# Kernel tuning notes

Measured on AMD Instinct MI355X. Metric: run time of the kernel, lower is better.

## Reference

```python
import jax, jax.numpy as jnp
import numpy as np

WIN = 11          # win_size
NC = 2            # num_classes
SMOOTH = 0.1      # smoothing / (num_classes - 1) = 0.1/1; fix_flag=True and 0.1 <= Max_Smootning=0.2


def setup_inputs() -> dict:
    key = jax.random.key(0)
    k1, k2 = jax.random.split(key)
    x = jax.random.normal(k1, (8, 2, 1024, 1024), dtype=jnp.float32)
    target = jax.random.randint(k2, (8, 1, 1024, 1024), 0, 2, dtype=jnp.int32)
    return {"x": x, "target": target}


def reference(x, target):
    kern = -jnp.ones((1, 1, WIN, WIN), dtype=jnp.float32)
    kern = kern.at[0, 0, WIN // 2, WIN // 2].set(float(WIN * WIN - 1))

    tf = target.astype(jnp.float32)  # [B,1,H,W]
    pad = WIN // 2
    edge = jax.lax.conv_general_dilated(tf, kern, window_strides=(1, 1),
                                        padding=[(pad, pad), (pad, pad)])
    edge = jnp.where(edge != 0, 1.0, 0.0)  # [B,1,H,W], 1 near label edges

    log_p = jax.nn.log_softmax(x, axis=1)  # [B,C,H,W]

    # One-hot masks (to_categorical with alpha=0 and alpha=smoothing).
    oh = jax.nn.one_hot(target[:, 0], NC, dtype=jnp.float32)  # [B,H,W,C]
    oh = jnp.transpose(oh, (0, 3, 1, 2))                      # [B,C,H,W]
    # alpha everywhere, 1 - alpha + alpha/NC at the true class
    soft = SMOOTH + oh * (1.0 - 2.0 * SMOOTH + SMOOTH / NC)

    mask = oh * (1.0 - edge) + soft * edge  # hard label off-edge, smoothed on-edge
    loss = jnp.mean(jnp.sum(mask * log_p, axis=1))
    return -loss
```

## Files before the change

### kernel.cpp

```cpp
#include <hip/hip_runtime.h>

#define HH 1024
#define WW 1024
#define BB 8
#define WORDS_X 16
#define NPART 2048

typedef unsigned long long u64;

__global__ __launch_bounds__(256) void ls_pack(const int* __restrict__ tgt,
                                               u64* __restrict__ bits) {
    const int lane = threadIdx.x & 63;
    const size_t wv = ((size_t)blockIdx.x * 256 + threadIdx.x) >> 6;
    const size_t wbase = wv * 8;
    const int* p = tgt + wbase * 64 + lane;

    int v[8];
#pragma unroll
    for (int j = 0; j < 8; ++j) v[j] = p[j * 64];

    u64 mine = 0;
#pragma unroll
    for (int j = 0; j < 8; ++j) {
        u64 m = __ballot(v[j] != 0);
        if (lane == j) mine = m;
    }
    if (lane < 8) bits[wbase + lane] = mine;
}

__global__ __launch_bounds__(256) void ls_loss(const float* __restrict__ x,
                                               const u64* __restrict__ bits,
                                               float* __restrict__ partial) {
    __shared__ u64 s_w[74][3];
    __shared__ u64 s_oh[74], s_ah[74], s_e[64];
    __shared__ float s_red[4];

    const int tid = threadIdx.x;
    const int b  = blockIdx.z;
    const int ty = blockIdx.y * 64;
    const int wx = blockIdx.x;

    if (tid < 222) {
        int r = tid / 3, k = tid - 3 * r;
        int gy = ty - 5 + r;
        int wi = wx - 1 + k;
        u64 v = 0;
        if ((unsigned)gy < HH && (unsigned)wi < WORDS_X)
            v = bits[((size_t)(b << 10) + gy) * WORDS_X + wi];
        s_w[r][k] = v;
    }

    const int row = tid >> 2;
    const int c0  = (tid & 3) << 4;
    const float* x0p = x + ((size_t)b * 2 + 0) * HH * WW
                         + (size_t)(ty + row) * WW + (wx << 6) + c0;
    const float* x1p = x0p + (size_t)HH * WW;
    float4 xv0[4], xv1[4];
#pragma unroll
    for (int q = 0; q < 4; ++q) xv0[q] = ((const float4*)x0p)[q];
#pragma unroll
    for (int q = 0; q < 4; ++q) xv1[q] = ((const float4*)x1p)[q];

    __syncthreads();

    if (tid < 74) {
        u64 wl = s_w[tid][0], wm = s_w[tid][1], wr = s_w[tid][2];
        u64 oh = wm, ah = wm;
#pragma unroll
        for (int d = 1; d <= 5; ++d) {
            u64 vr = (wm >> d) | (wr << (64 - d));
            u64 vl = (wm << d) | (wl >> (64 - d));
            oh |= vr | vl;
            ah &= vr & vl;
        }
        s_oh[tid] = oh;
        s_ah[tid] = ah;
    }
    __syncthreads();

    if (tid < 64) {
        u64 ov = 0, av = ~0ULL;
#pragma unroll
        for (int k = 0; k < 11; ++k) { ov |= s_oh[tid + k]; av &= s_ah[tid + k]; }
        u64 tc = s_w[tid + 5][1];
        s_e[tid] = (ov & ~tc) | (~av & tc);
    }
    __syncthreads();

    unsigned int e16 = (unsigned int)(s_e[row] >> c0) & 0xffffu;
    unsigned int t16 = (unsigned int)(s_w[row + 5][1] >> c0) & 0xffffu;

    const float* f0 = (const float*)xv0;
    const float* f1 = (const float*)xv1;
    float acc = 0.f;
#pragma unroll
    for (int j = 0; j < 16; ++j) {
        int t = (t16 >> j) & 1;
        int e = (e16 >> j) & 1;
        float v0 = f0[j], v1 = f1[j];
        float m   = fmaxf(v0, v1);
        float lse = m + __logf(1.0f + __expf(-fabsf(v0 - v1)));
        float lp0 = v0 - lse, lp1 = v1 - lse;
        float lpt = t ? lp1 : lp0;
        float lpo = t ? lp0 : lp1;
        acc += e ? (0.95f * lpt + 0.1f * lpo) : lpt;
    }

#pragma unroll
    for (int off = 32; off > 0; off >>= 1) acc += __shfl_down(acc, off, 64);
    if ((tid & 63) == 0) s_red[tid >> 6] = acc;
    __syncthreads();
    if (tid == 0) {
        int bid = (blockIdx.z * gridDim.y + blockIdx.y) * gridDim.x + blockIdx.x;
        partial[bid] = s_red[0] + s_red[1] + s_red[2] + s_red[3];
    }
}

__global__ __launch_bounds__(1024) void ls_final(const float* __restrict__ partial,
                                                 float* __restrict__ out) {
    __shared__ double s_red[16];
    const int tid = threadIdx.x;
    double s = (double)partial[tid] + (double)partial[tid + 1024];
#pragma unroll
    for (int off = 32; off > 0; off >>= 1) s += __shfl_down(s, off, 64);
    if ((tid & 63) == 0) s_red[tid >> 6] = s;
    __syncthreads();
    if (tid == 0) {
        double total = 0.0;
#pragma unroll
        for (int i = 0; i < 16; ++i) total += s_red[i];
        out[0] = (float)(-total * (1.0 / (8.0 * 1024.0 * 1024.0)));
    }
}

extern "C" void kernel_launch(void* const* d_in, const int* in_sizes, int n_in,
                              void* d_out, int out_size, void* d_ws, size_t ws_size,
                              hipStream_t stream) {
    const float* x  = (const float*)d_in[0];
    const int* tgt  = (const int*)d_in[1];

    float* partial = (float*)d_ws;
    u64* bits = (u64*)((char*)d_ws + (16 << 10));

    hipLaunchKernelGGL(ls_pack, dim3(4096), dim3(256), 0, stream, tgt, bits);
    hipLaunchKernelGGL(ls_loss, dim3(16, 16, 8), dim3(256), 0, stream, x, bits, partial);
    hipLaunchKernelGGL(ls_final, dim3(1), dim3(1024), 0, stream, partial, (float*)d_out);
}
```

Measured before the change: 119.3 us.

## Fuse target bit-packing into loss kernel, ballot halo rows directly from int targets

Result: slower. 128.6 us (+7.8%).

```diff
diff --git a/kernel.cpp b/kernel.cpp
--- a/kernel.cpp
+++ b/kernel.cpp
@@ -4,51 +4,22 @@
 #define WW 1024
 #define BB 8
 #define WORDS_X 16
-#define NPART 2048
 
 typedef unsigned long long u64;
 
-__global__ __launch_bounds__(256) void ls_pack(const int* __restrict__ tgt,
-                                               u64* __restrict__ bits) {
-    const int lane = threadIdx.x & 63;
-    const size_t wv = ((size_t)blockIdx.x * 256 + threadIdx.x) >> 6;
-    const size_t wbase = wv * 8;
-    const int* p = tgt + wbase * 64 + lane;
-
-    int v[8];
-#pragma unroll
-    for (int j = 0; j < 8; ++j) v[j] = p[j * 64];
-
-    u64 mine = 0;
-#pragma unroll
-    for (int j = 0; j < 8; ++j) {
-        u64 m = __ballot(v[j] != 0);
-        if (lane == j) mine = m;
-    }
-    if (lane < 8) bits[wbase + lane] = mine;
-}
-
-__global__ __launch_bounds__(256) void ls_loss(const float* __restrict__ x,
-                                               const u64* __restrict__ bits,
-                                               float* __restrict__ partial) {
+__global__ __launch_bounds__(256) void ls_fused(const float* __restrict__ x,
+                                                const int* __restrict__ tgt,
+                                                float* __restrict__ partial) {
     __shared__ u64 s_w[74][3];
     __shared__ u64 s_oh[74], s_ah[74], s_e[64];
     __shared__ float s_red[4];
 
-    const int tid = threadIdx.x;
+    const int tid  = threadIdx.x;
+    const int lane = tid & 63;
+    const int wave = tid >> 6;
     const int b  = blockIdx.z;
     const int ty = blockIdx.y * 64;
     const int wx = blockIdx.x;
-
-    if (tid < 222) {
-        int r = tid / 3, k = tid - 3 * r;
-        int gy = ty - 5 + r;
-        int wi = wx - 1 + k;
-        u64 v = 0;
-        if ((unsigned)gy < HH && (unsigned)wi < WORDS_X)
-            v = bits[((size_t)(b << 10) + gy) * WORDS_X + wi];
-        s_w[r][k] = v;
-    }
 
     const int row = tid >> 2;
     const int c0  = (tid & 3) << 4;
@@ -61,6 +32,24 @@
 #pragma unroll
     for (int q = 0; q < 4; ++q) xv1[q] = ((const float4*)x1p)[q];
 
+    const int* tb = tgt + ((size_t)b << 20);
+    for (int r = wave; r < 74; r += 4) {
+        const int gy = ty - 5 + r;
+        const bool rowok = ((unsigned)gy < HH);
+        const int* rp = tb + (size_t)(rowok ? gy : 0) * WW + lane;
+        u64 m[3];
+#pragma unroll
+        for (int k = 0; k < 3; ++k) {
+            const int wi = wx - 1 + k;
+            const bool valid = rowok & ((unsigned)wi < WORDS_X);
+            int v = rp[(valid ? wi : 0) << 6];
+            if (!valid) v = 0;
+            m[k] = __ballot(v != 0);
+        }
+        if (lane == 0) {
+            s_w[r][0] = m[0]; s_w[r][1] = m[1]; s_w[r][2] = m[2];
+        }
+    }
     __syncthreads();
 
     if (tid < 74) {
@@ -140,9 +129,7 @@
     const int* tgt  = (const int*)d_in[1];
 
     float* partial = (float*)d_ws;
-    u64* bits = (u64*)((char*)d_ws + (16 << 10));
 
-    hipLaunchKernelGGL(ls_pack, dim3(4096), dim3(256), 0, stream, tgt, bits);
-    hipLaunchKernelGGL(ls_loss, dim3(16, 16, 8), dim3(256), 0, stream, x, bits, partial);
+    hipLaunchKernelGGL(ls_fused, dim3(16, 16, 8), dim3(256), 0, stream, x, tgt, partial);
     hipLaunchKernelGGL(ls_final, dim3(1), dim3(1024), 0, stream, partial, (float*)d_out);
 }
```

## Split edge-mask computation into separate kernel before loss pass

Applied to the files above, without the earlier changes.

Measured after the change: 123.6 us. 1.04x slower.

```diff
diff --git a/kernel.cpp b/kernel.cpp
--- a/kernel.cpp
+++ b/kernel.cpp
@@ -4,7 +4,6 @@
 #define WW 1024
 #define BB 8
 #define WORDS_X 16
-#define NPART 2048
 
 typedef unsigned long long u64;
 
@@ -28,31 +27,66 @@
     if (lane < 8) bits[wbase + lane] = mine;
 }
 
-__global__ __launch_bounds__(256) void ls_loss(const float* __restrict__ x,
-                                               const u64* __restrict__ bits,
-                                               float* __restrict__ partial) {
-    __shared__ u64 s_w[74][3];
-    __shared__ u64 s_oh[74], s_ah[74], s_e[64];
+__global__ __launch_bounds__(256) void ls_edge(const u64* __restrict__ bits,
+                                               u64* __restrict__ ebits) {
+    __shared__ u64 s_b[26][17], s_oh[26][17], s_ah[26][17];
+    const int tid  = threadIdx.x;
+    const int slab = blockIdx.x;
+    const int b    = blockIdx.y;
+    const int y0   = slab << 4;
+
+#pragma unroll
+    for (int i = tid; i < 416; i += 256) {
+        int r = i >> 4, k = i & 15;
+        int gy = y0 - 5 + r;
+        u64 v = 0;
+        if ((unsigned)gy < HH) v = bits[((size_t)(b << 10) + gy) * WORDS_X + k];
+        s_b[r][k] = v;
+    }
+    __syncthreads();
+
+#pragma unroll
+    for (int i = tid; i < 416; i += 256) {
+        int r = i >> 4, k = i & 15;
+        u64 wm = s_b[r][k];
+        u64 wl = k ? s_b[r][k - 1] : 0;
+        u64 wr = (k < 15) ? s_b[r][k + 1] : 0;
+        u64 oh = wm, ah = wm;
+#pragma unroll
+        for (int d = 1; d <= 5; ++d) {
+            u64 vr = (wm >> d) | (wr << (64 - d));
+            u64 vl = (wm << d) | (wl >> (64 - d));
+            oh |= vr | vl;
+            ah &= vr & vl;
+        }
+        s_oh[r][k] = oh;
+        s_ah[r][k] = ah;
+    }
+    __syncthreads();
+
+    {
+        int r = tid >> 4, k = tid & 15;
+        u64 ov = 0, av = ~0ULL;
+#pragma unroll
+        for (int j = 0; j < 11; ++j) { ov |= s_oh[r + j][k]; av &= s_ah[r + j][k]; }
+        u64 tc = s_b[r + 5][k];
+        ebits[((size_t)(b << 10) + y0 + r) * WORDS_X + k] = (ov & ~tc) | (~av & tc);
+    }
+}
+
+__global__ __launch_bounds__(256) void ls_loss2(const float* __restrict__ x,
+                                                const u64* __restrict__ bits,
+                                                const u64* __restrict__ ebits,
+                                                float* __restrict__ partial) {
     __shared__ float s_red[4];
-
     const int tid = threadIdx.x;
     const int b  = blockIdx.z;
     const int ty = blockIdx.y * 64;
     const int wx = blockIdx.x;
-
-    if (tid < 222) {
-        int r = tid / 3, k = tid - 3 * r;
-        int gy = ty - 5 + r;
-        int wi = wx - 1 + k;
-        u64 v = 0;
-        if ((unsigned)gy < HH && (unsigned)wi < WORDS_X)
-            v = bits[((size_t)(b << 10) + gy) * WORDS_X + wi];
-        s_w[r][k] = v;
-    }
-
     const int row = tid >> 2;
     const int c0  = (tid & 3) << 4;
-    const float* x0p = x + ((size_t)b * 2 + 0) * HH * WW
+
+    const float* x0p = x + ((size_t)b * 2) * HH * WW
                          + (size_t)(ty + row) * WW + (wx << 6) + c0;
     const float* x1p = x0p + (size_t)HH * WW;
     float4 xv0[4], xv1[4];
@@ -61,34 +95,10 @@
 #pragma unroll
     for (int q = 0; q < 4; ++q) xv1[q] = ((const float4*)x1p)[q];
 
-    __syncthreads();
-
-    if (tid < 74) {
-        u64 wl = s_w[tid][0], wm = s_w[tid][1], wr = s_w[tid][2];
-        u64 oh = wm, ah = wm;
-#pragma unroll
-        for (int d = 1; d <= 5; ++d) {
-            u64 vr = (wm >> d) | (wr << (64 - d));
-            u64 vl = (wm << d) | (wl >> (64 - d));
-            oh |= vr | vl;
-            ah &= vr & vl;
-        }
-        s_oh[tid] = oh;
-        s_ah[tid] = ah;
-    }
-    __syncthreads();
-
-    if (tid < 64) {
-        u64 ov = 0, av = ~0ULL;
-#pragma unroll
-        for (int k = 0; k < 11; ++k) { ov |= s_oh[tid + k]; av &= s_ah[tid + k]; }
-        u64 tc = s_w[tid + 5][1];
-        s_e[tid] = (ov & ~tc) | (~av & tc);
-    }
-    __syncthreads();
-
-    unsigned int e16 = (unsigned int)(s_e[row] >> c0) & 0xffffu;
-    unsigned int t16 = (unsigned int)(s_w[row + 5][1] >> c0) & 0xffffu;
+    const size_t us = ((size_t)(b << 10) + ty + row) * (WORDS_X * 4)
+                    + (wx << 2) + (tid & 3);
+    const unsigned int t16 = ((const unsigned short*)bits)[us];
+    const unsigned int e16 = ((const unsigned short*)ebits)[us];
 
     const float* f0 = (const float*)xv0;
     const float* f1 = (const float*)xv1;
@@ -140,9 +150,12 @@
     const int* tgt  = (const int*)d_in[1];
 
     float* partial = (float*)d_ws;
-    u64* bits = (u64*)((char*)d_ws + (16 << 10));
+    u64* bits  = (u64*)((char*)d_ws + (16 << 10));
+    u64* ebits = (u64*)((char*)d_ws + (16 << 10) + (1 << 20));
 
     hipLaunchKernelGGL(ls_pack, dim3(4096), dim3(256), 0, stream, tgt, bits);
-    hipLaunchKernelGGL(ls_loss, dim3(16, 16, 8), dim3(256), 0, stream, x, bits, partial);
+    hipLaunchKernelGGL(ls_edge, dim3(64, 8), dim3(256), 0, stream, bits, ebits);
+    hipLaunchKernelGGL(ls_loss2, dim3(16, 16, 8), dim3(256), 0, stream,
+                       x, bits, ebits, partial);
     hipLaunchKernelGGL(ls_final, dim3(1), dim3(1024), 0, stream, partial, (float*)d_out);
 }
```
